# Kernel optimization log

Measured on AMD Instinct MI355X. Metric: run time of the kernel, lower is better.

Reference implementation:

```python
import jax, jax.numpy as jnp
import numpy as np
from jax import lax

DN = ('NCHW', 'OIHW', 'NCHW')
BN_EPS = 1e-5

def conv2d(x, w, b=None, pad=0):
    y = lax.conv_general_dilated(x, w, (1, 1), [(pad, pad), (pad, pad)], dimension_numbers=DN)
    if b is not None:
        y = y + b[None, :, None, None]
    return y

def setup_inputs() -> dict:
    key = jax.random.key(0)
    ks = jax.random.split(key, 12)
    B, C, H, W = 8, 256, 64, 64
    ca = C // 4  # dim_att = 64
    s = 0.05  # weight scale to keep attention logits sane
    return {
        'x': jax.random.normal(ks[0], (B, C, H, W), jnp.float32),
        'w_dw1': jax.random.normal(ks[1], (ca // 2, ca, 7, 7), jnp.float32) * s,
        'b_dw1': jax.random.normal(ks[2], (ca // 2,), jnp.float32) * s,
        'w_dw2': jax.random.normal(ks[3], (ca // 2, ca, 11, 11), jnp.float32) * s,
        'b_dw2': jax.random.normal(ks[4], (ca // 2,), jnp.float32) * s,
        'w_k': jax.random.normal(ks[5], (ca, ca, 1, 1), jnp.float32) * s,
        'b_k': jax.random.normal(ks[6], (ca,), jnp.float32) * s,
        'w_v': jax.random.normal(ks[7], (ca, ca, 1, 1), jnp.float32) * s,
        'b_v': jax.random.normal(ks[8], (ca,), jnp.float32) * s,
        'w_c1': jax.random.normal(ks[9], (C, C, 1, 1), jnp.float32) * s,
        'bn_g': jnp.ones((C,), jnp.float32),
        'bn_b': jnp.zeros((C,), jnp.float32),
        'bn_m': jnp.zeros((C,), jnp.float32),
        'bn_var': jnp.ones((C,), jnp.float32),
        'w_c2': jax.random.normal(ks[10], (C, C, 1, 1), jnp.float32) * s,
        'b_c2': jax.random.normal(ks[11], (C,), jnp.float32) * s,
    }

def reference(x, w_dw1, b_dw1, w_dw2, b_dw2, w_k, b_k, w_v, b_v,
              w_c1, bn_g, bn_b, bn_m, bn_var, w_c2, b_c2):
    ca = w_k.shape[0]  # dim_att
    B, C, H, W = x.shape
    HW = H * W
    x1 = x[:, :ca]
    x2 = x[:, ca:]
    # Q from two multi-scale convs (7x7 and 11x11, same padding)
    q = jnp.concatenate([conv2d(x1, w_dw1, b_dw1, pad=3),
                         conv2d(x1, w_dw2, b_dw2, pad=5)], axis=1)  # [B,ca,H,W]
    q = q.reshape(B, ca, HW)                                         # [B,ca,HW]
    k = conv2d(x1, w_k, b_k).reshape(B, ca, HW)                      # [B,ca,HW]
    v = conv2d(x1, w_v, b_v).reshape(B, ca, HW)                      # [B,ca,HW]
    # att[b,n,m] = softmax_m( sum_c q[b,c,n] * k[b,c,m] )
    att = jax.nn.softmax(jnp.einsum('bcn,bcm->bnm', q, k), axis=-1)  # [B,HW,HW]
    # out1[b,c,n] = sum_m v[b,c,m] * att[b,n,m]
    out1 = jnp.einsum('bcm,bnm->bcn', v, att).reshape(B, ca, H, W)
    y = jnp.concatenate([out1, x2], axis=1)  # [B,C,H,W]
    # conv1 = YOLO Conv: 1x1 conv (no bias) + BatchNorm (eval stats) + SiLU
    y = conv2d(y, w_c1)
    inv = lax.rsqrt(bn_var + BN_EPS)
    y = (y - bn_m[None, :, None, None]) * (bn_g * inv)[None, :, None, None] + bn_b[None, :, None, None]
    y = jax.nn.silu(y)
    # conv2 = plain 1x1 conv with bias
    return conv2d(y, w_c2, b_c2)
```

## Files before the change

### kernel.cpp

```cpp
#include <hip/hip_runtime.h>

typedef __attribute__((ext_vector_type(8))) short frag8;
typedef __attribute__((ext_vector_type(4))) float f32x4;
typedef __attribute__((ext_vector_type(8))) unsigned short us8;
typedef __attribute__((ext_vector_type(4))) unsigned short us4;
typedef __attribute__((ext_vector_type(2))) unsigned int u32x2;

#define MFMA(a,b,c) __builtin_amdgcn_mfma_f32_16x16x32_bf16((a),(b),(c),0,0,0)

__device__ __forceinline__ unsigned short f2bf(float f){
  unsigned int u = __builtin_bit_cast(unsigned int, f);
  u += 0x7fffu + ((u >> 16) & 1u);
  return (unsigned short)(u >> 16);
}

__device__ __forceinline__ float bf2f(unsigned short h){
  unsigned int u = ((unsigned int)h) << 16;
  return __builtin_bit_cast(float, u);
}

__device__ __forceinline__ unsigned int cvt_pk_bf16(float a, float b){
  unsigned int r;
  asm volatile("v_cvt_pk_bf16_f32 %0, %1, %2" : "=v"(r) : "v"(a), "v"(b));
  return r;
}

#define OFF_XT   ((size_t)0)
#define OFF_KT   ((size_t)16777216)
#define OFF_VCT  ((size_t)20971520)
#define OFF_QT   ((size_t)25165824)
#define OFF_O1T  ((size_t)29360128)
#define OFF_ZT   ((size_t)33554432)
#define OFF_WQ7  ((size_t)50331648)
#define OFF_WQ11 ((size_t)50532352)
#define OFF_WC1  ((size_t)51027968)
#define OFF_WC2  ((size_t)51159040)
#define OFF_BC1  ((size_t)51290112)
#define OFF_WKB  ((size_t)51291136)
#define OFF_WVB  ((size_t)51299328)
#define OFF_ML2  OFF_WQ7
#define OFF_ML4  ((size_t)51307520)
#define WS_NEED4 ((size_t)(OFF_ML4 + 1048576))

__global__ __launch_bounds__(256) void prep_weights_kernel(
    const float* __restrict__ wdw1, const float* __restrict__ wdw2,
    const float* __restrict__ wc1, const float* __restrict__ bng,
    const float* __restrict__ bnb, const float* __restrict__ bnm,
    const float* __restrict__ bnv, const float* __restrict__ wc2,
    const float* __restrict__ wk, const float* __restrict__ wv,
    unsigned short* __restrict__ wq7, unsigned short* __restrict__ wq11,
    unsigned short* __restrict__ wc1b, unsigned short* __restrict__ wc2b,
    float* __restrict__ bc1, unsigned short* __restrict__ wkb,
    unsigned short* __restrict__ wvb){
  int i = blockIdx.x*256 + threadIdx.x;
  if (i < 100352){
    int o = i >> 11, rem = i & 2047;
    int co = rem >> 6, ci = rem & 63;
    int kh = o / 7, kw = o % 7;
    wq7[i] = f2bf(wdw1[(co*64 + ci)*49 + kh*7 + kw]);
  } else if (i < 348160){
    int j = i - 100352;
    int o = j >> 11, rem = j & 2047;
    int co = rem >> 6, ci = rem & 63;
    int kh = o / 11, kw = o % 11;
    wq11[j] = f2bf(wdw2[(co*64 + ci)*121 + kh*11 + kw]);
  } else if (i < 413696){
    int j = i - 348160;
    int co = j >> 8;
    float a = bng[co] * rsqrtf(bnv[co] + 1e-5f);
    wc1b[j] = f2bf(wc1[j] * a);
    if ((j & 255) == 0) bc1[co] = bnb[co] - bnm[co]*a;
  } else if (i < 479232){
    int j = i - 413696;
    wc2b[j] = f2bf(wc2[j]);
  } else if (i < 483328){
    int j = i - 479232;
    wkb[j] = f2bf(wk[j]);
  } else if (i < 487424){
    int j = i - 483328;
    wvb[j] = f2bf(wv[j]);
  }
}

__global__ __launch_bounds__(256) void prep_x_kernel(const float* __restrict__ x,
                                                     unsigned short* __restrict__ xt){
  int g = blockIdx.x*256 + threadIdx.x;
  int b = g >> 12, n = g & 4095;
  int c0base = blockIdx.y * 64;
  const float* xp = x + (((size_t)b*256) << 12) + n;
  unsigned short* op = xt + (size_t)g*256;
  for (int c0 = c0base; c0 < c0base + 64; c0 += 8){
    us8 v;
    #pragma unroll
    for (int j = 0; j < 8; ++j) v[j] = f2bf(xp[(size_t)(c0+j) << 12]);
    *reinterpret_cast<us8*>(op + c0) = v;
  }
}

__global__ __launch_bounds__(256) void kv_kernel(const unsigned short* __restrict__ xt,
    const unsigned short* __restrict__ wkb, const unsigned short* __restrict__ wvb,
    const float* __restrict__ bk, const float* __restrict__ bv,
    unsigned short* __restrict__ kt, unsigned short* __restrict__ vct){
  int gid = blockIdx.x;
  int part = gid >> 9, t = gid & 511;
  int b = t >> 6, tile = t & 63;
  int lane = threadIdx.x & 63, wid = threadIdx.x >> 6;
  int lo = lane & 15, hi = lane >> 4;
  int n0 = tile*64 + wid*16;
  size_t bb = (size_t)b << 12;
  f32x4 acc[4];
  #pragma unroll
  for (int f = 0; f < 4; ++f) acc[f] = (f32x4){0.f,0.f,0.f,0.f};
  frag8 x0 = *reinterpret_cast<const frag8*>(xt + (bb + n0 + lo)*256 + 8*hi);
  frag8 x1 = *reinterpret_cast<const frag8*>(xt + (bb + n0 + lo)*256 + 32 + 8*hi);
  if (part == 0){
    #pragma unroll
    for (int nf = 0; nf < 4; ++nf){
      frag8 w0 = *reinterpret_cast<const frag8*>(wkb + (nf*16 + lo)*64 + 8*hi);
      frag8 w1 = *reinterpret_cast<const frag8*>(wkb + (nf*16 + lo)*64 + 32 + 8*hi);
      acc[nf] = MFMA(x0, w0, acc[nf]);
      acc[nf] = MFMA(x1, w1, acc[nf]);
    }
    #pragma unroll
    for (int nf = 0; nf < 4; ++nf){
      int co = nf*16 + lo;
      float bias = bk[co];
      #pragma unroll
      for (int r = 0; r < 4; ++r)
        kt[(bb + n0 + hi*4 + r)*64 + co] = f2bf(acc[nf][r] + bias);
    }
  } else {
    #pragma unroll
    for (int mf = 0; mf < 4; ++mf){
      frag8 w0 = *reinterpret_cast<const frag8*>(wvb + (mf*16 + lo)*64 + 8*hi);
      frag8 w1 = *reinterpret_cast<const frag8*>(wvb + (mf*16 + lo)*64 + 32 + 8*hi);
      acc[mf] = MFMA(w0, x0, acc[mf]);
      acc[mf] = MFMA(w1, x1, acc[mf]);
    }
    #pragma unroll
    for (int mf = 0; mf < 4; ++mf){
      #pragma unroll
      for (int r = 0; r < 4; ++r){
        int c = mf*16 + hi*4 + r;
        vct[(((size_t)b*64 + c) << 12) + n0 + lo] = f2bf(acc[mf][r] + bv[c]);
      }
    }
  }
}

template<int KS>
__global__ __launch_bounds__(256) void conv_q_kernel(const unsigned short* __restrict__ xt,
    const unsigned short* __restrict__ wq, const float* __restrict__ bias,
    unsigned short* __restrict__ qt){
  constexpr int P = KS/2;
  __shared__ unsigned short xs[(P+1)*64*64];
  __shared__ float outst[64*33];
  int h = blockIdx.x, b = blockIdx.y;
  int tid = threadIdx.x, lane = tid & 63, wid = tid >> 6;
  int lo = lane & 15, hi = lane >> 4;
  int cofrag = wid & 1, nhalf = wid >> 1;
  f32x4 acc[2] = {{0.f,0.f,0.f,0.f},{0.f,0.f,0.f,0.f}};
  const size_t xbase = ((size_t)b << 12) * 256;
  #pragma unroll
  for (int pass = 0; pass < 2; ++pass){
    const int nrows = pass ? P : (P+1);
    const int srcBase = pass ? (h+1) : (h-P);
    const int dhBase = pass ? (P+1) : 0;
    if (pass) __syncthreads();
    for (int idx = tid; idx < nrows*512; idx += 256){
      int rl = idx >> 9, w = (idx >> 3) & 63, ch = idx & 7;
      int sr = srcBase + rl;
      us8 v = {0,0,0,0,0,0,0,0};
      if (sr >= 0 && sr < 64)
        v = *reinterpret_cast<const us8*>(xt + xbase + (size_t)(sr*64 + w)*256 + ch*8);
      int byte = (rl*64 + w)*128 + ((ch*16) ^ ((w & 7) << 4));
      *reinterpret_cast<us8*>((char*)xs + byte) = v;
    }
    __syncthreads();
    for (int dh = 0; dh < nrows; ++dh){
      frag8 wf[KS][2];
      int off0 = (dhBase + dh)*KS;
      #pragma unroll
      for (int dw = 0; dw < KS; ++dw){
        #pragma unroll
        for (int ks = 0; ks < 2; ++ks)
          wf[dw][ks] = *reinterpret_cast<const frag8*>(
              wq + (size_t)(off0+dw)*2048 + (cofrag*16 + lo)*64 + ks*32 + 8*hi);
      }
      #pragma unroll
      for (int dw = 0; dw < KS; ++dw){
        #pragma unroll
        for (int nf = 0; nf < 2; ++nf){
          int w_out = nhalf*32 + nf*16 + lo;
          int wp = w_out + dw - P;
          frag8 bx0 = {0,0,0,0,0,0,0,0}, bx1 = {0,0,0,0,0,0,0,0};
          if (wp >= 0 && wp < 64){
            int rowb = (dh*64 + wp)*128;
            int sw = (wp & 7) << 4;
            bx0 = *reinterpret_cast<const frag8*>((char*)xs + rowb + ((hi*16) ^ sw));
            bx1 = *reinterpret_cast<const frag8*>((char*)xs + rowb + ((64 + hi*16) ^ sw));
          }
          acc[nf] = MFMA(wf[dw][0], bx0, acc[nf]);
          acc[nf] = MFMA(wf[dw][1], bx1, acc[nf]);
        }
      }
    }
  }
  __syncthreads();
  #pragma unroll
  for (int nf = 0; nf < 2; ++nf){
    int w = nhalf*32 + nf*16 + lo;
    #pragma unroll
    for (int r = 0; r < 4; ++r){
      int co = cofrag*16 + hi*4 + r;
      outst[w*33 + co] = acc[nf][r];
    }
  }
  __syncthreads();
  {
    int w = tid >> 2, c8 = (tid & 3)*8;
    int cobase = (KS == 7) ? 0 : 32;
    us8 v;
    #pragma unroll
    for (int j = 0; j < 8; ++j) v[j] = f2bf(outst[w*33 + c8 + j] + bias[c8 + j]);
    *reinterpret_cast<us8*>(qt + (((size_t)b << 12) + h*64 + w)*64 + cobase + c8) = v;
  }
}

template<int NSPLIT>
__global__ __launch_bounds__(256, 2) void attn_kernel(const unsigned short* __restrict__ qt,
    const unsigned short* __restrict__ kt, const unsigned short* __restrict__ vct,
    unsigned short* __restrict__ opart, float* __restrict__ mlpart){
  constexpr int TILES = 64 / NSPLIT;
  __shared__ unsigned short kls[2][64*64];
  __shared__ unsigned short vls[2][64*64];
  __shared__ unsigned short pls[4][32*64];
  int b = blockIdx.y, half = blockIdx.z;
  int tid = threadIdx.x, lane = tid & 63, wid = tid >> 6;
  int lo = lane & 15, hi = lane >> 4;
  int q0 = blockIdx.x*128 + wid*32;
  const size_t bb = (size_t)b << 12;
  const int mtbase = half * TILES;
  const int sm = tid >> 3, sch = tid & 7;
  const int dstA = sm*128 + ((sch*16) ^ ((sm & 7) << 4));
  const int dstB = dstA + 32*128;
  char* pbase = (char*)pls[wid];
  frag8 aq[2][2];
  #pragma unroll
  for (int mf = 0; mf < 2; ++mf)
    #pragma unroll
    for (int ks = 0; ks < 2; ++ks)
      aq[mf][ks] = *reinterpret_cast<const frag8*>(
          qt + (bb + q0 + mf*16 + lo)*64 + ks*32 + 8*hi);
  f32x4 o[2][4];
  #pragma unroll
  for (int mf = 0; mf < 2; ++mf)
    #pragma unroll
    for (int f = 0; f < 4; ++f) o[mf][f] = (f32x4){0.f,0.f,0.f,0.f};
  float mr[2]  = {-1e30f, -1e30f};
  float lr[2]  = {0.f, 0.f};
  float mrT[2][4];
  #pragma unroll
  for (int mf = 0; mf < 2; ++mf)
    #pragma unroll
    for (int r = 0; r < 4; ++r) mrT[mf][r] = -1e30f;
  us8 kr0, kr1, vr0, vr1;
  {
    int mt = mtbase;
    kr0 = *reinterpret_cast<const us8*>(kt + (bb + mt*64 + sm)*64 + sch*8);
    kr1 = *reinterpret_cast<const us8*>(kt + (bb + mt*64 + sm + 32)*64 + sch*8);
    vr0 = *reinterpret_cast<const us8*>(vct + (((size_t)b*64 + sm) << 12) + mt*64 + sch*8);
    vr1 = *reinterpret_cast<const us8*>(vct + (((size_t)b*64 + sm + 32) << 12) + mt*64 + sch*8);
    *reinterpret_cast<us8*>((char*)kls[0] + dstA) = kr0;
    *reinterpret_cast<us8*>((char*)kls[0] + dstB) = kr1;
    *reinterpret_cast<us8*>((char*)vls[0] + dstA) = vr0;
    *reinterpret_cast<us8*>((char*)vls[0] + dstB) = vr1;
  }
  __syncthreads();
  int cur = 0;
  for (int t = 0; t < TILES; ++t){
    if (t < TILES-1){
      int mt = mtbase + t + 1;
      kr0 = *reinterpret_cast<const us8*>(kt + (bb + mt*64 + sm)*64 + sch*8);
      kr1 = *reinterpret_cast<const us8*>(kt + (bb + mt*64 + sm + 32)*64 + sch*8);
      vr0 = *reinterpret_cast<const us8*>(vct + (((size_t)b*64 + sm) << 12) + mt*64 + sch*8);
      vr1 = *reinterpret_cast<const us8*>(vct + (((size_t)b*64 + sm + 32) << 12) + mt*64 + sch*8);
    }
    f32x4 s[2][4];
    #pragma unroll
    for (int mf = 0; mf < 2; ++mf)
      #pragma unroll
      for (int f = 0; f < 4; ++f) s[mf][f] = (f32x4){0.f,0.f,0.f,0.f};
    #pragma unroll
    for (int nf = 0; nf < 4; ++nf){
      int m = nf*16 + lo;
      int sw = (m & 7) << 4;
      frag8 b0 = *reinterpret_cast<const frag8*>((char*)kls[cur] + m*128 + ((hi*16) ^ sw));
      frag8 b1 = *reinterpret_cast<const frag8*>((char*)kls[cur] + m*128 + ((64 + hi*16) ^ sw));
      s[0][nf] = MFMA(b0, aq[0][0], s[0][nf]);
      s[0][nf] = MFMA(b1, aq[0][1], s[0][nf]);
      s[1][nf] = MFMA(b0, aq[1][0], s[1][nf]);
      s[1][nf] = MFMA(b1, aq[1][1], s[1][nf]);
    }
    float pm[2];
    #pragma unroll
    for (int mf = 0; mf < 2; ++mf){
      float a0 = fmaxf(fmaxf(s[mf][0][0], s[mf][0][1]), fmaxf(s[mf][0][2], s[mf][0][3]));
      float a1 = fmaxf(fmaxf(s[mf][1][0], s[mf][1][1]), fmaxf(s[mf][1][2], s[mf][1][3]));
      float a2 = fmaxf(fmaxf(s[mf][2][0], s[mf][2][1]), fmaxf(s[mf][2][2], s[mf][2][3]));
      float a3 = fmaxf(fmaxf(s[mf][3][0], s[mf][3][1]), fmaxf(s[mf][3][2], s[mf][3][3]));
      pm[mf] = fmaxf(fmaxf(a0, a1), fmaxf(a2, a3));
    }
    float growth = fmaxf(pm[0] - mr[0], pm[1] - mr[1]);
    if (!__all(growth <= 8.0f)){
      float rmax[2] = {pm[0], pm[1]};
      #pragma unroll
      for (int mf = 0; mf < 2; ++mf){
        rmax[mf] = fmaxf(rmax[mf], __shfl_xor(rmax[mf], 16));
        rmax[mf] = fmaxf(rmax[mf], __shfl_xor(rmax[mf], 32));
        float mn = fmaxf(mr[mf], rmax[mf]);
        lr[mf] *= __expf(mr[mf] - mn);
        mr[mf] = mn;
      }
      #pragma unroll
      for (int mf = 0; mf < 2; ++mf)
        #pragma unroll
        for (int r = 0; r < 4; ++r){
          float mnT = __shfl(mr[mf], hi*4 + r);
          float scT = __expf(mrT[mf][r] - mnT);
          mrT[mf][r] = mnT;
          #pragma unroll
          for (int nf = 0; nf < 4; ++nf) o[mf][nf][r] *= scT;
        }
    }
    #pragma unroll
    for (int mf = 0; mf < 2; ++mf){
      float acc = 0.f;
      #pragma unroll
      for (int nf = 0; nf < 4; ++nf){
        #pragma unroll
        for (int r = 0; r < 4; ++r){
          s[mf][nf][r] = __expf(s[mf][nf][r] - mr[mf]);
          acc += s[mf][nf][r];
        }
        u32x2 w;
        w[0] = cvt_pk_bf16(s[mf][nf][0], s[mf][nf][1]);
        w[1] = cvt_pk_bf16(s[mf][nf][2], s[mf][nf][3]);
        *reinterpret_cast<u32x2*>(pbase + (mf*16 + lo)*128 +
            ((nf*32 + hi*8) ^ ((lo & 7) << 4))) = w;
      }
      lr[mf] += acc;
    }
    #pragma unroll
    for (int ks = 0; ks < 2; ++ks){
      frag8 ap0 = *reinterpret_cast<const frag8*>(
          pbase + lo*128 + ((ks*64 + hi*16) ^ ((lo & 7) << 4)));
      frag8 ap1 = *reinterpret_cast<const frag8*>(
          pbase + (16 + lo)*128 + ((ks*64 + hi*16) ^ ((lo & 7) << 4)));
      #pragma unroll
      for (int nf = 0; nf < 4; ++nf){
        int c = nf*16 + lo;
        frag8 bv = *reinterpret_cast<const frag8*>(
            (char*)vls[cur] + c*128 + ((ks*64 + hi*16) ^ ((c & 7) << 4)));
        o[0][nf] = MFMA(ap0, bv, o[0][nf]);
        o[1][nf] = MFMA(ap1, bv, o[1][nf]);
      }
    }
    if (t < TILES-1){
      *reinterpret_cast<us8*>((char*)kls[cur^1] + dstA) = kr0;
      *reinterpret_cast<us8*>((char*)kls[cur^1] + dstB) = kr1;
      *reinterpret_cast<us8*>((char*)vls[cur^1] + dstA) = vr0;
      *reinterpret_cast<us8*>((char*)vls[cur^1] + dstB) = vr1;
    }
    __syncthreads();
    cur ^= 1;
  }
  #pragma unroll
  for (int mf = 0; mf < 2; ++mf){
    lr[mf] += __shfl_xor(lr[mf], 16);
    lr[mf] += __shfl_xor(lr[mf], 32);
  }
  size_t pb = ((size_t)(half*8 + b) << 12);
  #pragma unroll
  for (int mf = 0; mf < 2; ++mf){
    #pragma unroll
    for (int nf = 0; nf < 4; ++nf)
      #pragma unroll
      for (int r = 0; r < 4; ++r)
        opart[(pb + q0 + mf*16 + hi*4 + r)*64 + nf*16 + lo] = f2bf(o[mf][nf][r]);
    if (hi == 0){
      size_t idx = pb + q0 + mf*16 + lo;
      mlpart[idx*2]     = mr[mf];
      mlpart[idx*2 + 1] = lr[mf];
    }
  }
}

template<int NSPLIT>
__global__ __launch_bounds__(256) void merge_kernel(const unsigned short* __restrict__ opart,
    const float* __restrict__ mlpart, unsigned short* __restrict__ o1t){
  int g = blockIdx.x*256 + threadIdx.x;
  int c4 = g & 15, q = (g >> 4) & 4095, b = g >> 16;
  size_t idx[NSPLIT];
  float m[NSPLIT], l[NSPLIT];
  float M = -1e30f;
  #pragma unroll
  for (int p = 0; p < NSPLIT; ++p){
    idx[p] = ((size_t)(p*8 + b) << 12) + q;
    m[p] = mlpart[idx[p]*2];
    l[p] = mlpart[idx[p]*2 + 1];
    M = fmaxf(M, m[p]);
  }
  float denom = 0.f, w[NSPLIT];
  #pragma unroll
  for (int p = 0; p < NSPLIT; ++p){
    w[p] = __expf(m[p] - M);
    denom += w[p] * l[p];
  }
  float inv = 1.0f / denom;
  f32x4 acc = (f32x4){0.f,0.f,0.f,0.f};
  #pragma unroll
  for (int p = 0; p < NSPLIT; ++p){
    us4 a = *reinterpret_cast<const us4*>(opart + idx[p]*64 + c4*4);
    float wp = w[p] * inv;
    #pragma unroll
    for (int j = 0; j < 4; ++j) acc[j] += wp * bf2f(a[j]);
  }
  unsigned short outv[4];
  #pragma unroll
  for (int j = 0; j < 4; ++j) outv[j] = f2bf(acc[j]);
  *reinterpret_cast<ulonglong1*>(o1t + (((size_t)b << 12) + q)*64 + c4*4) =
      *reinterpret_cast<ulonglong1*>(outv);
}

__global__ __launch_bounds__(256) void c1_kernel(const unsigned short* __restrict__ o1t,
    const unsigned short* __restrict__ xt, const unsigned short* __restrict__ wc1b,
    const float* __restrict__ bc1, unsigned short* __restrict__ zt){
  int b = blockIdx.y;
  int q0 = blockIdx.x*64 + (threadIdx.x >> 6)*16;
  int lane = threadIdx.x & 63, lo = lane & 15, hi = lane >> 4;
  size_t bb = (size_t)b << 12;
  f32x4 acc[16];
  #pragma unroll
  for (int nf = 0; nf < 16; ++nf) acc[nf] = (f32x4){0.f,0.f,0.f,0.f};
  #pragma unroll
  for (int ks = 0; ks < 8; ++ks){
    int ci0 = ks*32 + 8*hi;
    frag8 a;
    if (ks < 2) a = *reinterpret_cast<const frag8*>(o1t + (bb + q0 + lo)*64 + ci0);
    else        a = *reinterpret_cast<const frag8*>(xt  + (bb + q0 + lo)*256 + ci0);
    #pragma unroll
    for (int nf = 0; nf < 16; ++nf){
      frag8 w = *reinterpret_cast<const frag8*>(wc1b + (nf*16 + lo)*256 + ci0);
      acc[nf] = MFMA(a, w, acc[nf]);
    }
  }
  #pragma unroll
  for (int nf = 0; nf < 16; ++nf){
    int co = nf*16 + lo;
    float bias = bc1[co];
    #pragma unroll
    for (int r = 0; r < 4; ++r){
      float y = acc[nf][r] + bias;
      y = y / (1.0f + __expf(-y));
      zt[(bb + q0 + hi*4 + r)*256 + co] = f2bf(y);
    }
  }
}

__global__ __launch_bounds__(256) void c2_kernel(const unsigned short* __restrict__ zt,
    const unsigned short* __restrict__ wc2b, const float* __restrict__ bc2,
    float* __restrict__ out){
  int b = blockIdx.y;
  int q0 = blockIdx.x*128 + (threadIdx.x >> 6)*32;
  int lane = threadIdx.x & 63, lo = lane & 15, hi = lane >> 4;
  size_t bb = (size_t)b << 12;
  f32x4 acc[16][2];
  #pragma unroll
  for (int mf = 0; mf < 16; ++mf){
    acc[mf][0] = (f32x4){0.f,0.f,0.f,0.f};
    acc[mf][1] = (f32x4){0.f,0.f,0.f,0.f};
  }
  #pragma unroll
  for (int ks = 0; ks < 8; ++ks){
    int ci0 = ks*32 + 8*hi;
    frag8 bz0 = *reinterpret_cast<const frag8*>(zt + (bb + q0 + lo)*256 + ci0);
    frag8 bz1 = *reinterpret_cast<const frag8*>(zt + (bb + q0 + 16 + lo)*256 + ci0);
    #pragma unroll
    for (int mf = 0; mf < 16; ++mf){
      frag8 aw = *reinterpret_cast<const frag8*>(wc2b + (mf*16 + lo)*256 + ci0);
      acc[mf][0] = MFMA(aw, bz0, acc[mf][0]);
      acc[mf][1] = MFMA(aw, bz1, acc[mf][1]);
    }
  }
  #pragma unroll
  for (int mf = 0; mf < 16; ++mf){
    #pragma unroll
    for (int r = 0; r < 4; ++r){
      int co = mf*16 + hi*4 + r;
      float bias = bc2[co];
      float* op = out + (((size_t)b*256 + co) << 12) + q0 + lo;
      op[0]  = acc[mf][0][r] + bias;
      op[16] = acc[mf][1][r] + bias;
    }
  }
}

extern "C" void kernel_launch(void* const* d_in, const int* in_sizes, int n_in,
                              void* d_out, int out_size, void* d_ws, size_t ws_size,
                              hipStream_t stream){
  const float* x    = (const float*)d_in[0];
  const float* wdw1 = (const float*)d_in[1];
  const float* bdw1 = (const float*)d_in[2];
  const float* wdw2 = (const float*)d_in[3];
  const float* bdw2 = (const float*)d_in[4];
  const float* wk   = (const float*)d_in[5];
  const float* bk   = (const float*)d_in[6];
  const float* wv   = (const float*)d_in[7];
  const float* bv   = (const float*)d_in[8];
  const float* wc1  = (const float*)d_in[9];
  const float* bng  = (const float*)d_in[10];
  const float* bnb  = (const float*)d_in[11];
  const float* bnm  = (const float*)d_in[12];
  const float* bnv  = (const float*)d_in[13];
  const float* wc2  = (const float*)d_in[14];
  const float* bc2  = (const float*)d_in[15];
  char* ws = (char*)d_ws;
  unsigned short* xt   = (unsigned short*)(ws + OFF_XT);
  unsigned short* ktp  = (unsigned short*)(ws + OFF_KT);
  unsigned short* vct  = (unsigned short*)(ws + OFF_VCT);
  unsigned short* qtp  = (unsigned short*)(ws + OFF_QT);
  unsigned short* o1t  = (unsigned short*)(ws + OFF_O1T);
  unsigned short* zt   = (unsigned short*)(ws + OFF_ZT);
  unsigned short* wq7  = (unsigned short*)(ws + OFF_WQ7);
  unsigned short* wq11 = (unsigned short*)(ws + OFF_WQ11);
  unsigned short* wc1b = (unsigned short*)(ws + OFF_WC1);
  unsigned short* wc2b = (unsigned short*)(ws + OFF_WC2);
  float*          bc1  = (float*)(ws + OFF_BC1);
  unsigned short* wkb  = (unsigned short*)(ws + OFF_WKB);
  unsigned short* wvb  = (unsigned short*)(ws + OFF_WVB);
  unsigned short* opart = (unsigned short*)(ws + OFF_ZT);
  const bool big = (ws_size >= WS_NEED4);
  float*          mlp   = (float*)(ws + (big ? OFF_ML4 : OFF_ML2));

  prep_weights_kernel<<<1904, 256, 0, stream>>>(wdw1, wdw2, wc1, bng, bnb, bnm, bnv,
                                                wc2, wk, wv, wq7, wq11, wc1b, wc2b,
                                                bc1, wkb, wvb);
  prep_x_kernel<<<dim3(128, 4), 256, 0, stream>>>(x, xt);
  kv_kernel<<<1024, 256, 0, stream>>>(xt, wkb, wvb, bk, bv, ktp, vct);
  conv_q_kernel<7><<<dim3(64, 8), 256, 0, stream>>>(xt, wq7, bdw1, qtp);
  conv_q_kernel<11><<<dim3(64, 8), 256, 0, stream>>>(xt, wq11, bdw2, qtp);
  if (big){
    attn_kernel<4><<<dim3(32, 8, 4), 256, 0, stream>>>(qtp, ktp, vct, opart, mlp);
    merge_kernel<4><<<2048, 256, 0, stream>>>(opart, mlp, o1t);
  } else {
    attn_kernel<2><<<dim3(32, 8, 2), 256, 0, stream>>>(qtp, ktp, vct, opart, mlp);
    merge_kernel<2><<<2048, 256, 0, stream>>>(opart, mlp, o1t);
  }
  c1_kernel<<<dim3(64, 8), 256, 0, stream>>>(o1t, xt, wc1b, bc1, zt);
  c2_kernel<<<dim3(32, 8), 256, 0, stream>>>(zt, wc2b, bc2, (float*)d_out);
}
```

Measured before the change: 260.0 us.

## Compute two output rows per conv_q block to share staged input rows

Each conv_q block now produces two adjacent output rows. Each wave pair handles one row across the full width, and the staged input window is shared between them. This cuts redundant global loads and LDS staging of the input halo rows by nearly half. In exchange the grid has half as many blocks (256 per kernel), there are more accumulators per wave, and waves skip kernel rows that fall outside their window. That skipping can leave some waves idle in each pass.

```diff
diff --git a/kernel.cpp b/kernel.cpp
--- a/kernel.cpp
+++ b/kernel.cpp
@@ -153,21 +153,23 @@
     const unsigned short* __restrict__ wq, const float* __restrict__ bias,
     unsigned short* __restrict__ qt){
   constexpr int P = KS/2;
-  __shared__ unsigned short xs[(P+1)*64*64];
-  __shared__ float outst[64*33];
-  int h = blockIdx.x, b = blockIdx.y;
+  constexpr int NR = (KS+1)/2;
+  __shared__ unsigned short xs[NR*64*64];
+  __shared__ float outst[2][64][33];
+  int h0 = blockIdx.x*2, b = blockIdx.y;
   int tid = threadIdx.x, lane = tid & 63, wid = tid >> 6;
   int lo = lane & 15, hi = lane >> 4;
-  int cofrag = wid & 1, nhalf = wid >> 1;
-  f32x4 acc[2] = {{0.f,0.f,0.f,0.f},{0.f,0.f,0.f,0.f}};
+  int cofrag = wid & 1, hsel = wid >> 1;
+  int h = h0 + hsel;
+  f32x4 acc[4];
+  #pragma unroll
+  for (int nf = 0; nf < 4; ++nf) acc[nf] = (f32x4){0.f,0.f,0.f,0.f};
   const size_t xbase = ((size_t)b << 12) * 256;
   #pragma unroll
   for (int pass = 0; pass < 2; ++pass){
-    const int nrows = pass ? P : (P+1);
-    const int srcBase = pass ? (h+1) : (h-P);
-    const int dhBase = pass ? (P+1) : 0;
+    const int srcBase = h0 - P + pass*NR;
     if (pass) __syncthreads();
-    for (int idx = tid; idx < nrows*512; idx += 256){
+    for (int idx = tid; idx < NR*512; idx += 256){
       int rl = idx >> 9, w = (idx >> 3) & 63, ch = idx & 7;
       int sr = srcBase + rl;
       us8 v = {0,0,0,0,0,0,0,0};
@@ -177,9 +179,11 @@
       *reinterpret_cast<us8*>((char*)xs + byte) = v;
     }
     __syncthreads();
-    for (int dh = 0; dh < nrows; ++dh){
+    for (int rl = 0; rl < NR; ++rl){
+      int dh = srcBase + rl - h + P;
+      if (dh < 0 || dh >= KS) continue;
       frag8 wf[KS][2];
-      int off0 = (dhBase + dh)*KS;
+      int off0 = dh*KS;
       #pragma unroll
       for (int dw = 0; dw < KS; ++dw){
         #pragma unroll
@@ -190,12 +194,12 @@
       #pragma unroll
       for (int dw = 0; dw < KS; ++dw){
         #pragma unroll
-        for (int nf = 0; nf < 2; ++nf){
-          int w_out = nhalf*32 + nf*16 + lo;
+        for (int nf = 0; nf < 4; ++nf){
+          int w_out = nf*16 + lo;
           int wp = w_out + dw - P;
           frag8 bx0 = {0,0,0,0,0,0,0,0}, bx1 = {0,0,0,0,0,0,0,0};
           if (wp >= 0 && wp < 64){
-            int rowb = (dh*64 + wp)*128;
+            int rowb = (rl*64 + wp)*128;
             int sw = (wp & 7) << 4;
             bx0 = *reinterpret_cast<const frag8*>((char*)xs + rowb + ((hi*16) ^ sw));
             bx1 = *reinterpret_cast<const frag8*>((char*)xs + rowb + ((64 + hi*16) ^ sw));
@@ -206,24 +210,27 @@
       }
     }
   }
-  __syncthreads();
-  #pragma unroll
-  for (int nf = 0; nf < 2; ++nf){
-    int w = nhalf*32 + nf*16 + lo;
-    #pragma unroll
-    for (int r = 0; r < 4; ++r){
-      int co = cofrag*16 + hi*4 + r;
-      outst[w*33 + co] = acc[nf][r];
-    }
+  #pragma unroll
+  for (int nf = 0; nf < 4; ++nf){
+    int w = nf*16 + lo;
+    #pragma unroll
+    for (int r = 0; r < 4; ++r)
+      outst[hsel][w][cofrag*16 + hi*4 + r] = acc[nf][r];
   }
   __syncthreads();
   {
-    int w = tid >> 2, c8 = (tid & 3)*8;
+    int hs = tid >> 7, rem = tid & 127;
+    int w = rem >> 1, c16 = (rem & 1)*16;
     int cobase = (KS == 7) ? 0 : 32;
-    us8 v;
-    #pragma unroll
-    for (int j = 0; j < 8; ++j) v[j] = f2bf(outst[w*33 + c8 + j] + bias[c8 + j]);
-    *reinterpret_cast<us8*>(qt + (((size_t)b << 12) + h*64 + w)*64 + cobase + c8) = v;
+    size_t qrow = (((size_t)b << 12) + (h0 + hs)*64 + w)*64;
+    #pragma unroll
+    for (int g = 0; g < 2; ++g){
+      int c8 = c16 + g*8;
+      us8 v;
+      #pragma unroll
+      for (int j = 0; j < 8; ++j) v[j] = f2bf(outst[hs][w][c8 + j] + bias[c8 + j]);
+      *reinterpret_cast<us8*>(qt + qrow + cobase + c8) = v;
+    }
   }
 }
 
@@ -548,8 +555,8 @@
                                                 bc1, wkb, wvb);
   prep_x_kernel<<<dim3(128, 4), 256, 0, stream>>>(x, xt);
   kv_kernel<<<1024, 256, 0, stream>>>(xt, wkb, wvb, bk, bv, ktp, vct);
-  conv_q_kernel<7><<<dim3(64, 8), 256, 0, stream>>>(xt, wq7, bdw1, qtp);
-  conv_q_kernel<11><<<dim3(64, 8), 256, 0, stream>>>(xt, wq11, bdw2, qtp);
+  conv_q_kernel<7><<<dim3(32, 8), 256, 0, stream>>>(xt, wq7, bdw1, qtp);
+  conv_q_kernel<11><<<dim3(32, 8), 256, 0, stream>>>(xt, wq11, bdw2, qtp);
   if (big){
     attn_kernel<4><<<dim3(32, 8, 4), 256, 0, stream>>>(qtp, ktp, vct, opart, mlp);
     merge_kernel<4><<<2048, 256, 0, stream>>>(opart, mlp, o1t);
```

Result: faster. 233.2 us (-10.3%).
